# Kernel optimization log

Hardware: AMD Instinct MI355X
Metric: run time of the kernel (lower is better)

The kernel has to match this reference:

```python
import jax, jax.numpy as jnp
import numpy as np
from math import sqrt

B, S, E, H = 2, 2048, 768, 12
DH = E // H
W = 256            # one-sided attention window (attention_window=512)
G = 16             # number of global tokens (positions 0..G-1 in every batch row)
PAD = 128          # last PAD tokens per row are padding (masked)
FF = 3072          # SwiGLU intermediate size
NEG = -1e9
EPS = 1e-5


def _ln(x, g, b):
    m = jnp.mean(x, axis=-1, keepdims=True)
    v = jnp.var(x, axis=-1, keepdims=True)
    return (x - m) * jax.lax.rsqrt(v + EPS) * g + b


def _rope(x, t):
    # x: [B,H,S,DH]; t: [B,S] float 'set positions'
    half = DH // 2
    inv_freq = 1.0 / (10000.0 ** (jnp.arange(half, dtype=jnp.float32) / half))
    ang = t[:, None, :, None] * inv_freq            # [B,1,S,half]
    cos, sin = jnp.cos(ang), jnp.sin(ang)
    x1, x2 = x[..., :half], x[..., half:]
    return jnp.concatenate([x1 * cos - x2 * sin, x2 * cos + x1 * sin], axis=-1)


def _heads(x):  # [B,S,E] -> [B,H,S,DH]
    return x.reshape(B, S, H, DH).transpose(0, 2, 1, 3)


def _chunk3(x):
    # [B,H,S,D] -> [B,H,C,3W,D]: for query chunk c, keys from chunks c-1,c,c+1 (zero padded)
    b, h, s, d = x.shape
    c = s // W
    xp = jnp.pad(x, ((0, 0), (0, 0), (W, W), (0, 0))).reshape(b, h, c + 2, W, d)
    return jnp.concatenate([xp[:, :, :-2], xp[:, :, 1:-1], xp[:, :, 2:]], axis=3)


def _forward(x, attention_mask, global_attention_mask,
             Wq, bq, Wk, bk, Wv, bv, Wqg, bqg, Wkg, bkg, Wvg, bvg,
             ln0_g, ln0_b, ln1_g, ln1_b, W1, W3, W2):
    C = S // W
    merged = attention_mask * (global_attention_mask + 1)   # 0 masked, 1 local, 2 global
    is_masked = merged == 0
    is_global = merged == 2
    remove = merged != 1   # keys removed from windowed attention (masked or global)

    q = _heads(x @ Wq + bq) / sqrt(DH)
    k = _heads(x @ Wk + bk)
    v = _heads(x @ Wv + bv)

    # RoPE over 'set positions': (~is_index_masked) * cumsum(is_index_global_attn)
    t = jnp.where(is_masked, 0, jnp.cumsum(is_global.astype(jnp.int32), axis=1)).astype(jnp.float32)
    q = _rope(q, t)
    k = _rope(k, t)

    # --- sliding-window (banded) scores: band[b,h,i,d] = q_i . k_{i+d-W} ---
    qc = q.reshape(B, H, C, W, DH)
    k3 = _chunk3(k)
    s3 = jnp.einsum('bhcpd,bhcqd->bhcpq', qc, k3)                     # [B,H,C,W,3W]
    didx = jnp.arange(W)[:, None] + jnp.arange(2 * W + 1)[None, :]    # [W,2W+1]
    band = jnp.take_along_axis(s3, didx[None, None, None], axis=-1)   # [B,H,C,W,2W+1]

    # mask removed keys / out-of-range positions inside the band
    rmp = jnp.pad(remove, ((0, 0), (W, W)), constant_values=True).reshape(B, C + 2, W)
    rm3 = jnp.concatenate([rmp[:, :-2], rmp[:, 1:-1], rmp[:, 2:]], axis=2)  # [B,C,3W]
    band_rm = jnp.take_along_axis(jnp.broadcast_to(rm3[:, :, None, :], (B, C, W, 3 * W)),
                                  didx[None, None], axis=-1)                # [B,C,W,2W+1]
    band = jnp.where(band_rm[:, None], NEG, band).reshape(B, H, S, 2 * W + 1)

    # --- global-key columns (keys taken from the RoPE'd local key vectors) ---
    sg = jnp.einsum('bhid,bhgd->bhig', q, k[:, :, :G])                # [B,H,S,G]

    scores = jnp.concatenate([sg, band], axis=-1)                     # [B,H,S,G+2W+1]
    probs = jax.nn.softmax(scores.astype(jnp.float32), axis=-1).astype(x.dtype)
    probs = jnp.where(is_masked[:, None, :, None], 0.0, probs)

    # --- probs @ value: global columns + band ---
    out = jnp.einsum('bhig,bhgd->bhid', probs[..., :G], v[:, :, :G])
    pl = probs[..., G:].reshape(B, H, C, W, 2 * W + 1)
    rows = jnp.broadcast_to(jnp.arange(W)[:, None], (W, 2 * W + 1))
    p3 = jnp.zeros((B, H, C, W, 3 * W), probs.dtype).at[:, :, :, rows, didx].set(pl)
    v3 = _chunk3(v)
    out = out + jnp.einsum('bhcpq,bhcqd->bhcpd', p3, v3).reshape(B, H, S, DH)
    attn = out.transpose(0, 2, 1, 3).reshape(B, S, E)

    # --- full attention for global tokens (separate global projections, no RoPE) ---
    gq = _heads(x @ Wqg + bqg)[:, :, :G] / sqrt(DH)                   # [B,H,G,DH]
    gk = _heads(x @ Wkg + bkg)
    gv = _heads(x @ Wvg + bvg)
    gs = jnp.einsum('bhgd,bhjd->bhgj', gq, gk)                        # [B,H,G,S]
    gs = jnp.where(is_masked[:, None, None, :], NEG, gs)
    gp = jax.nn.softmax(gs.astype(jnp.float32), axis=-1).astype(x.dtype)
    gout = jnp.einsum('bhgj,bhjd->bhgd', gp, gv).transpose(0, 2, 1, 3).reshape(B, G, E)
    attn = attn.at[:, :G].set(gout)

    # residual + post-LN, SwiGLU FFN, residual + post-LN (dropout = eval mode)
    h0 = _ln(x + attn, ln0_g, ln0_b)
    ffn = (jax.nn.silu(h0 @ W1) * (h0 @ W3)) @ W2
    return _ln(h0 + ffn, ln1_g, ln1_b)


def setup_inputs():
    key = jax.random.key(0)
    ks = jax.random.split(key, 12)
    x = jax.random.normal(ks[0], (B, S, E), jnp.float32)
    attention_mask = jnp.ones((B, S), jnp.int32).at[:, S - PAD:].set(0)
    global_attention_mask = jnp.zeros((B, S), jnp.int32).at[:, :G].set(1)
    sd = 0.02
    def w(k, shape):
        return jax.random.normal(k, shape, jnp.float32) * sd
    return dict(
        x=x, attention_mask=attention_mask, global_attention_mask=global_attention_mask,
        Wq=w(ks[1], (E, E)), bq=jnp.zeros((E,), jnp.float32),
        Wk=w(ks[2], (E, E)), bk=jnp.zeros((E,), jnp.float32),
        Wv=w(ks[3], (E, E)), bv=jnp.zeros((E,), jnp.float32),
        Wqg=w(ks[4], (E, E)), bqg=jnp.zeros((E,), jnp.float32),
        Wkg=w(ks[5], (E, E)), bkg=jnp.zeros((E,), jnp.float32),
        Wvg=w(ks[6], (E, E)), bvg=jnp.zeros((E,), jnp.float32),
        ln0_g=jnp.ones((E,), jnp.float32), ln0_b=jnp.zeros((E,), jnp.float32),
        ln1_g=jnp.ones((E,), jnp.float32), ln1_b=jnp.zeros((E,), jnp.float32),
        W1=w(ks[7], (E, FF)), W3=w(ks[8], (E, FF)), W2=w(ks[9], (FF, E)))


def reference(x, attention_mask, global_attention_mask, Wq, bq, Wk, bk, Wv, bv,
              Wqg, bqg, Wkg, bkg, Wvg, bvg, ln0_g, ln0_b, ln1_g, ln1_b, W1, W3, W2):
    return _forward(x, attention_mask, global_attention_mask,
                    Wq, bq, Wk, bk, Wv, bv, Wqg, bqg, Wkg, bkg, Wvg, bvg,
                    ln0_g, ln0_b, ln1_g, ln1_b, W1, W3, W2)
```

## Files before the change

kernel.cpp:

```cpp
#include <hip/hip_runtime.h>


#define BB_ 2
#define SS 2048
#define EE 768
#define HH 12
#define DHH 64
#define GG 16
#define FFN 3072
#define MM (BB_*SS)

typedef __bf16 bf16_t;
typedef __bf16 bf16x8_t __attribute__((ext_vector_type(8)));
typedef float f32x4_t __attribute__((ext_vector_type(4)));

__device__ inline void gload16(const void* g, void* l) {
  __builtin_amdgcn_global_load_lds((const __attribute__((address_space(1))) void*)g,
                                   (__attribute__((address_space(3))) void*)l, 16, 0, 0);
}

__global__ __launch_bounds__(64) void detect_kernel(const unsigned int* __restrict__ w,
                                                    int* __restrict__ flag) {
  int cnt = 0;
  for (int i = threadIdx.x; i < 1024; i += 64) {
    unsigned e = (w[i] >> 7) & 0xFF;
    cnt += (e >= 100 && e <= 144) ? 1 : 0;
  }
  for (int off = 32; off; off >>= 1) cnt += __shfl_xor(cnt, off);
  if (threadIdx.x == 0) flag[0] = (cnt > 512) ? 1 : 0;
}

struct CanonP { const void* src[11]; bf16_t* dst[11]; };

__global__ __launch_bounds__(256) void canon_kernel(CanonP P, const int* __restrict__ flag) {
  constexpr int ns[11] = {3145728, 768,768,768,768,768,768, 768,768,768,768};
  int idx4 = (blockIdx.x*256 + threadIdx.x)*4;
  const bool isb = flag[0] != 0;
  int off = 0, seg = -1, loc = 0;
  #pragma unroll
  for (int i=0;i<11;i++) {
    if (seg < 0 && idx4 < off + ns[i]) { seg = i; loc = idx4 - off; }
    off += ns[i];
  }
  if (seg < 0) return;
  const void* s = P.src[seg];
  bf16_t* d = P.dst[seg];
  if (isb) {
    *(uint2*)&d[loc] = *(const uint2*)((const unsigned short*)s + loc);
  } else {
    float4 v = *(const float4*)((const float*)s + loc);
    d[loc+0] = (bf16_t)v.x; d[loc+1] = (bf16_t)v.y;
    d[loc+2] = (bf16_t)v.z; d[loc+3] = (bf16_t)v.w;
  }
}

struct TP6 { const void* s[6]; bf16_t* d[6]; };

__global__ __launch_bounds__(256) void trans_kernel(TP6 P, int R, int C,
                                                    const int* __restrict__ flag) {
  const int z = blockIdx.z;
  const void* src = P.s[z]; bf16_t* dst = P.d[z];
  const bool isb = flag[0] != 0;
  __shared__ bf16_t tile[32][33];
  int tx = threadIdx.x & 31, ty = threadIdx.x >> 5;
  int r0 = blockIdx.y*32, c0 = blockIdx.x*32;
  #pragma unroll
  for (int i=0;i<4;i++) {
    int rr = ty + i*8;
    size_t si = (size_t)(r0+rr)*C + c0 + tx;
    tile[rr][tx] = isb ? ((const bf16_t*)src)[si] : (bf16_t)((const float*)src)[si];
  }
  __syncthreads();
  #pragma unroll
  for (int i=0;i<4;i++) {
    int cc = ty + i*8;
    dst[(size_t)(c0+cc)*R + r0 + tx] = tile[tx][cc];
  }
}

__global__ __launch_bounds__(256) void flags_kernel(const int* __restrict__ am,
                                                    const int* __restrict__ gm,
                                                    float* __restrict__ tpos,
                                                    int* __restrict__ flags,
                                                    float* __restrict__ zbuf,
                                                    int zn) {
  int blk = blockIdx.x;
  if (blk >= BB_) {
    int i = (blk - BB_)*256 + threadIdx.x;
    if (i < zn) zbuf[i] = 0.f;
    return;
  }
  int b = blk;
  int t = threadIdx.x;
  int lane = t & 63, wv = t >> 6;
  int base = b*SS + t*8;
  int mg[8]; int isg[8]; int loc = 0;
  for (int i=0;i<8;i++) {
    int a = am[base+i], g = gm[base+i];
    int merged = a*(g+1);
    mg[i] = merged;
    isg[i] = (merged==2) ? 1 : 0;
    loc += isg[i];
  }
  int x = loc;
  for (int off=1; off<64; off<<=1) {
    int y = __shfl_up(x, off);
    if (lane >= off) x += y;
  }
  __shared__ int wtot[4];
  if (lane==63) wtot[wv] = x;
  __syncthreads();
  int prev = 0;
  for (int w=0; w<wv; w++) prev += wtot[w];
  int run = prev + x - loc;
  for (int i=0;i<8;i++) {
    run += isg[i];
    int masked = (mg[i]==0) ? 1 : 0;
    int glob   = (mg[i]==2) ? 1 : 0;
    int rem    = (mg[i]!=1) ? 1 : 0;
    tpos[base+i]  = masked ? 0.f : (float)run;
    flags[base+i] = masked | (glob<<1) | (rem<<2);
  }
}

__device__ inline void gemm128_core(const bf16_t* __restrict__ A,
                                    const bf16_t* __restrict__ BT,
                                    int ldA, int ldB, int kbeg, int kend,
                                    int m0, int n0,
                                    bf16_t* As, bf16_t* Bs,
                                    f32x4_t (&acc)[4][4]) {
  const int t = threadIdx.x;
  const int lane = t & 63, wv = t >> 6;
  const int l15 = lane & 15, quad = lane >> 4;
  const int wr = (wv >> 1) << 6, wc = (wv & 1) << 6;
  const int rsub = lane >> 3, pch = lane & 7;
  const int sch = pch ^ rsub;
  const size_t abase = (size_t)(m0 + wv*32 + rsub)*ldA + sch*8;
  const size_t bbase = (size_t)(n0 + wv*32 + rsub)*ldB + sch*8;
  const int sx = l15 & 7;
  bf16_t* lA = As + (wv*32)*64;
  bf16_t* lB = Bs + (wv*32)*64;
  for (int k0 = kbeg; k0 < kend; k0 += 64) {
    __syncthreads();
    #pragma unroll
    for (int j=0;j<4;j++) {
      gload16(A + abase + (size_t)(j*8)*ldA + k0, lA + j*8*64);
      gload16(BT + bbase + (size_t)(j*8)*ldB + k0, lB + j*8*64);
    }
    __syncthreads();
    #pragma unroll
    for (int c=0;c<2;c++) {
      bf16x8_t af[4], bfr[4];
      #pragma unroll
      for (int a=0;a<4;a++)
        af[a] = *(const bf16x8_t*)&As[(wr + a*16 + l15)*64 + ((c*4+quad)^sx)*8];
      #pragma unroll
      for (int b=0;b<4;b++)
        bfr[b] = *(const bf16x8_t*)&Bs[(wc + b*16 + l15)*64 + ((c*4+quad)^sx)*8];
      #pragma unroll
      for (int a=0;a<4;a++)
        #pragma unroll
        for (int b=0;b<4;b++)
          acc[a][b] = __builtin_amdgcn_mfma_f32_16x16x32_bf16(af[a], bfr[b], acc[a][b], 0,0,0);
    }
  }
}

struct ProjParams {
  const bf16_t* W[5];
  const bf16_t* Bi[5];
  bf16_t* O[5];
};

__global__ __launch_bounds__(256) void proj_kernel(const bf16_t* __restrict__ x,
                                                   ProjParams P,
                                                   const float* __restrict__ tpos) {
  const int m0 = blockIdx.x*128, n0 = blockIdx.y*128;
  const int z  = blockIdx.z;
  __shared__ bf16_t As[128*64];
  __shared__ bf16_t Bs[128*64];
  f32x4_t acc[4][4];
  #pragma unroll
  for (int a=0;a<4;a++)
    #pragma unroll
    for (int b=0;b<4;b++) acc[a][b] = (f32x4_t){0.f,0.f,0.f,0.f};
  gemm128_core(x, P.W[z], EE, EE, 0, EE, m0, n0, As, Bs, acc);

  const int t = threadIdx.x;
  const int lane = t & 63, wv = t >> 6;
  const int l15 = lane & 15, quad = lane >> 4;
  const int wr = (wv >> 1) << 6, wc = (wv & 1) << 6;
  const float scale = (z==0) ? 0.125f : 1.f;
  const bool rope = (z<2);
  const int h = (n0 + wc) >> 6;
  bf16_t* Oz = P.O[z];
  const bf16_t* Bz = P.Bi[z];
  float bvals[4];
  #pragma unroll
  for (int b=0;b<4;b++) bvals[b] = (float)Bz[h*64 + b*16 + l15];
  #pragma unroll
  for (int a=0;a<4;a++) {
    #pragma unroll
    for (int r=0;r<4;r++) {
      int row = m0 + wr + a*16 + quad*4 + r;
      int bb = row >> 11, spos = row & (SS-1);
      float vals[4];
      #pragma unroll
      for (int b=0;b<4;b++) vals[b] = (acc[a][b][r] + bvals[b]) * scale;
      if (rope) {
        float tv = tpos[row];
        #pragma unroll
        for (int b=0;b<2;b++) {
          int j = b*16 + l15;
          float inv = __expf(-(float)j * (9.210340371976184f/32.f));
          float ang = tv * inv;
          float sn = __sinf(ang), cs = __cosf(ang);
          float x1 = vals[b], x2 = vals[b+2];
          vals[b]   = x1*cs - x2*sn;
          vals[b+2] = x2*cs + x1*sn;
        }
      }
      bf16_t* dst = Oz + ((size_t)(bb*HH + h)*SS + spos)*DHH;
      #pragma unroll
      for (int b=0;b<4;b++) dst[b*16 + l15] = (bf16_t)vals[b];
    }
  }
}

__global__ __launch_bounds__(256) void gemm_ffn13(const bf16_t* __restrict__ A,
                                                  const bf16_t* __restrict__ B1T,
                                                  const bf16_t* __restrict__ B3T,
                                                  bf16_t* __restrict__ g1) {
  const int n0 = blockIdx.x*64, m0 = blockIdx.y*128;
  __shared__ bf16_t As[128*64];
  __shared__ bf16_t Bs1[64*64];
  __shared__ bf16_t Bs3[64*64];
  const int t = threadIdx.x;
  const int lane = t & 63, wv = t >> 6;
  const int l15 = lane & 15, quad = lane >> 4;
  const int wr = (wv >> 1) << 6, wc = (wv & 1) << 5;
  const int rsub = lane >> 3, pch = lane & 7;
  const int sch = pch ^ rsub;
  const size_t abase = (size_t)(m0 + wv*32 + rsub)*EE + sch*8;
  const size_t bbase = (size_t)(n0 + wv*16 + rsub)*EE + sch*8;
  const int sx = l15 & 7;
  bf16_t* lA  = As  + (wv*32)*64;
  bf16_t* lB1 = Bs1 + (wv*16)*64;
  bf16_t* lB3 = Bs3 + (wv*16)*64;
  f32x4_t a1[4][2], a3[4][2];
  #pragma unroll
  for (int a=0;a<4;a++)
    #pragma unroll
    for (int b=0;b<2;b++) { a1[a][b] = (f32x4_t){0.f,0.f,0.f,0.f};
                            a3[a][b] = (f32x4_t){0.f,0.f,0.f,0.f}; }
  for (int k0 = 0; k0 < EE; k0 += 64) {
    __syncthreads();
    #pragma unroll
    for (int j=0;j<4;j++)
      gload16(A + abase + (size_t)(j*8)*EE + k0, lA + j*8*64);
    #pragma unroll
    for (int j=0;j<2;j++) {
      gload16(B1T + bbase + (size_t)(j*8)*EE + k0, lB1 + j*8*64);
      gload16(B3T + bbase + (size_t)(j*8)*EE + k0, lB3 + j*8*64);
    }
    __syncthreads();
    #pragma unroll
    for (int c=0;c<2;c++) {
      bf16x8_t af[4], b1f[2], b3f[2];
      #pragma unroll
      for (int a=0;a<4;a++)
        af[a] = *(const bf16x8_t*)&As[(wr + a*16 + l15)*64 + ((c*4+quad)^sx)*8];
      #pragma unroll
      for (int b=0;b<2;b++) {
        b1f[b] = *(const bf16x8_t*)&Bs1[(wc + b*16 + l15)*64 + ((c*4+quad)^sx)*8];
        b3f[b] = *(const bf16x8_t*)&Bs3[(wc + b*16 + l15)*64 + ((c*4+quad)^sx)*8];
      }
      #pragma unroll
      for (int a=0;a<4;a++)
        #pragma unroll
        for (int b=0;b<2;b++) {
          a1[a][b] = __builtin_amdgcn_mfma_f32_16x16x32_bf16(af[a], b1f[b], a1[a][b], 0,0,0);
          a3[a][b] = __builtin_amdgcn_mfma_f32_16x16x32_bf16(af[a], b3f[b], a3[a][b], 0,0,0);
        }
    }
  }
  #pragma unroll
  for (int a=0;a<4;a++)
    #pragma unroll
    for (int r=0;r<4;r++) {
      int row = m0 + wr + a*16 + quad*4 + r;
      #pragma unroll
      for (int b=0;b<2;b++) {
        float tv = a1[a][b][r];
        float sil = tv / (1.f + __expf(-tv));
        g1[(size_t)row*FFN + n0 + wc + b*16 + l15] = (bf16_t)(sil * a3[a][b][r]);
      }
    }
}

struct Ffn2Out { float* p[4]; };

__global__ __launch_bounds__(256) void gemm_ffn2(const bf16_t* __restrict__ A,
                                                 const bf16_t* __restrict__ BT,
                                                 Ffn2Out O) {
  const int m0 = blockIdx.x*128, n0 = blockIdx.y*128;
  const int kz = blockIdx.z;
  __shared__ bf16_t As[128*64];
  __shared__ bf16_t Bs[128*64];
  f32x4_t acc[4][4];
  #pragma unroll
  for (int a=0;a<4;a++)
    #pragma unroll
    for (int b=0;b<4;b++) acc[a][b] = (f32x4_t){0.f,0.f,0.f,0.f};
  gemm128_core(A, BT, FFN, FFN, kz*768, (kz+1)*768, m0, n0, As, Bs, acc);
  const int t = threadIdx.x;
  const int lane = t & 63, wv = t >> 6;
  const int l15 = lane & 15, quad = lane >> 4;
  const int wr = (wv >> 1) << 6, wc = (wv & 1) << 6;
  float* C = O.p[kz];
  #pragma unroll
  for (int a=0;a<4;a++)
    #pragma unroll
    for (int r=0;r<4;r++) {
      int row = m0 + wr + a*16 + quad*4 + r;
      #pragma unroll
      for (int b=0;b<4;b++)
        C[(size_t)row*EE + n0 + wc + b*16 + l15] = acc[a][b][r];
    }
}

__global__ __launch_bounds__(64) void qg_kernel(const bf16_t* __restrict__ x,
                                                const bf16_t* __restrict__ WqgT,
                                                const bf16_t* __restrict__ bqg,
                                                float* __restrict__ qgb) {
  int g = blockIdx.x, h = blockIdx.y, b = blockIdx.z;
  int d = threadIdx.x;
  __shared__ float xs[EE];
  for (int i=d; i<EE; i+=64) xs[i] = (float)x[((size_t)b*SS + g)*EE + i];
  __syncthreads();
  float acc = 0.f;
  const bf16_t* wrow = WqgT + (size_t)(h*64+d)*EE;
  #pragma unroll 4
  for (int k=0;k<EE;k+=8) {
    bf16x8_t w8 = *(const bf16x8_t*)(wrow + k);
    #pragma unroll
    for (int i=0;i<8;i++) acc += xs[k+i] * (float)w8[i];
  }
  acc = (acc + (float)bqg[h*64+d]) * 0.125f;
  qgb[((size_t)(b*HH+h)*GG + g)*DHH + d] = acc;
}

__global__ __launch_bounds__(256) void band_kernel(const bf16_t* __restrict__ qb,
                                                   const bf16_t* __restrict__ kb,
                                                   const bf16_t* __restrict__ vb,
                                                   const int* __restrict__ flags,
                                                   float* __restrict__ attn) {
  const int flat = blockIdx.x;
  const int nb = (flat & 7) * 48 + (flat >> 3);
  const int px = nb & 15;
  const int hb = nb >> 4;
  const int h = hb % HH, b = hb / HH;
  const int p0 = px * 128;

  const int t = threadIdx.x;
  const int wv = t>>6, lane = t&63;
  const int l15 = lane & 15, quad = lane >> 4;
  const size_t bh = (size_t)(b*HH+h);
  const bf16_t* kbh = kb + bh*SS*DHH;
  const bf16_t* vbh = vb + bh*SS*DHH;
  const int* fl = flags + b*SS;
  const int qbase = p0 + wv*32;

  __shared__ bf16_t Ks[2][64*DHH];
  __shared__ bf16_t Vt[2][64*72];
  __shared__ bf16_t Pw[4][32*72];

  bf16x8_t qa[2][2];
  #pragma unroll
  for (int g=0; g<2; g++) {
    const bf16_t* qrow = qb + (bh*SS + qbase + g*16 + l15)*DHH;
    qa[g][0] = *(const bf16x8_t*)(qrow + quad*8);
    qa[g][1] = *(const bf16x8_t*)(qrow + 32 + quad*8);
  }

  const int srsub = lane >> 3, spch = lane & 7;
  const int vkp  = (t & 31) * 2;
  const int vdh0 = (t >> 5) * 8;

  {
    const int kb0 = p0 - 256;
    #pragma unroll
    for (int j=0;j<2;j++) {
      int row = wv*16 + j*8 + srsub;
      int kc = min(max(kb0 + row, 0), SS-1);
      gload16(kbh + (size_t)kc*DHH + (spch ^ srsub)*8, &Ks[0][(wv*16 + j*8)*DHH]);
    }
    int kc1 = min(max(kb0 + vkp,   0), SS-1);
    int kc2 = min(max(kb0 + vkp+1, 0), SS-1);
    bf16x8_t v1 = *(const bf16x8_t*)(vbh + (size_t)kc1*DHH + vdh0);
    bf16x8_t v2 = *(const bf16x8_t*)(vbh + (size_t)kc2*DHH + vdh0);
    #pragma unroll
    for (int i=0;i<8;i++) {
      union { unsigned u; bf16_t hh[2]; } pk;
      pk.hh[0] = v1[i]; pk.hh[1] = v2[i];
      *(unsigned*)&Vt[0][(vdh0+i)*72 + vkp] = pk.u;
    }
  }
  __syncthreads();

  f32x4_t o[2][4];
  #pragma unroll
  for (int g=0; g<2; g++)
    #pragma unroll
    for (int i=0;i<4;i++) o[g][i] = (f32x4_t){0.f,0.f,0.f,0.f};
  float lsum[2][4] = {{0.f,0.f,0.f,0.f},{0.f,0.f,0.f,0.f}};
  bf16_t* P = Pw[wv];

  for (int unit=0; unit<11; unit++) {
    const int cur = unit & 1, nxt = cur ^ 1;
    const int kb0 = (unit<10) ? (p0 - 256 + unit*64) : 0;
    const bool pre = (unit < 10);
    bf16x8_t pv1, pv2;
    if (pre) {
      const int kbn = (unit < 9) ? (kb0 + 64) : 0;
      #pragma unroll
      for (int j=0;j<2;j++) {
        int row = wv*16 + j*8 + srsub;
        int kc = min(max(kbn + row, 0), SS-1);
        gload16(kbh + (size_t)kc*DHH + (spch ^ srsub)*8, &Ks[nxt][(wv*16 + j*8)*DHH]);
      }
      int kc1 = min(max(kbn + vkp,   0), SS-1);
      int kc2 = min(max(kbn + vkp+1, 0), SS-1);
      pv1 = *(const bf16x8_t*)(vbh + (size_t)kc1*DHH + vdh0);
      pv2 = *(const bf16x8_t*)(vbh + (size_t)kc2*DHH + vdh0);
    }
    const bf16_t* Kc = Ks[cur];
    const int nsub = (unit<10) ? 4 : 1;
    for (int sub=0; sub<4; sub++) {
      if (sub < nsub) {
        int krow = sub*16 + l15;
        int kpos = kb0 + krow;
        bf16x8_t kf0 = *(const bf16x8_t*)&Kc[krow*DHH + (((quad  ) ^ (krow&7))<<3)];
        bf16x8_t kf1 = *(const bf16x8_t*)&Kc[krow*DHH + (((quad+4) ^ (krow&7))<<3)];
        int kc = min(max(kpos,0),SS-1);
        bool drop = false;
        if (unit<10) drop = (kpos<0) || (kpos>=SS) || (((fl[kc]>>2)&1)!=0);
        #pragma unroll
        for (int g=0; g<2; g++) {
          f32x4_t s = (f32x4_t){0.f,0.f,0.f,0.f};
          s = __builtin_amdgcn_mfma_f32_16x16x32_bf16(qa[g][0], kf0, s, 0,0,0);
          s = __builtin_amdgcn_mfma_f32_16x16x32_bf16(qa[g][1], kf1, s, 0,0,0);
          #pragma unroll
          for (int r=0;r<4;r++) {
            float e;
            if (unit==10) {
              e = __expf(s[r]);
            } else {
              int dj = kpos - (qbase + g*16 + quad*4 + r);
              bool valid = (dj>=-256) && (dj<=256) && (!drop);
              e = valid ? __expf(s[r]) : 0.f;
            }
            lsum[g][r] += e;
            P[(g*16 + quad*4 + r)*72 + sub*16 + l15] = (bf16_t)e;
          }
        }
      } else {
        #pragma unroll
        for (int g=0; g<2; g++)
          #pragma unroll
          for (int r=0;r<4;r++) P[(g*16 + quad*4 + r)*72 + sub*16 + l15] = (bf16_t)0.f;
      }
    }
    __builtin_amdgcn_s_setprio(1);
    #pragma unroll
    for (int g=0; g<2; g++) {
      #pragma unroll
      for (int chunk=0; chunk<2; chunk++) {
        bf16x8_t pf = *(const bf16x8_t*)&P[(g*16 + l15)*72 + chunk*32 + quad*8];
        #pragma unroll
        for (int nt=0; nt<4; nt++) {
          bf16x8_t vf = *(const bf16x8_t*)&Vt[cur][(nt*16+l15)*72 + chunk*32 + quad*8];
          o[g][nt] = __builtin_amdgcn_mfma_f32_16x16x32_bf16(pf, vf, o[g][nt], 0,0,0);
        }
      }
    }
    __builtin_amdgcn_s_setprio(0);
    if (pre) {
      #pragma unroll
      for (int i=0;i<8;i++) {
        union { unsigned u; bf16_t hh[2]; } pk;
        pk.hh[0] = pv1[i]; pk.hh[1] = pv2[i];
        *(unsigned*)&Vt[nxt][(vdh0+i)*72 + vkp] = pk.u;
      }
      __syncthreads();
    }
  }
  #pragma unroll
  for (int g=0; g<2; g++) {
    #pragma unroll
    for (int r=0;r<4;r++) {
      float s = lsum[g][r];
      s += __shfl_xor(s,1); s += __shfl_xor(s,2);
      s += __shfl_xor(s,4); s += __shfl_xor(s,8);
      lsum[g][r] = s;
    }
    #pragma unroll
    for (int r=0;r<4;r++) {
      int q = qbase + g*16 + quad*4 + r;
      int masked = fl[q] & 1;
      float inv = masked ? 0.f : 1.f/lsum[g][r];
      float* dst = attn + ((size_t)(b*SS+q))*EE + h*64 + l15;
      #pragma unroll
      for (int nt=0; nt<4; nt++) dst[nt*16] = o[g][nt][r]*inv;
    }
  }
}

__global__ __launch_bounds__(256) void gattn_part(const float* __restrict__ qgb,
                                                  const bf16_t* __restrict__ kgb,
                                                  const bf16_t* __restrict__ vgb,
                                                  const int* __restrict__ flags,
                                                  float* __restrict__ go,
                                                  float* __restrict__ gl) {
  const int kbase = blockIdx.x*128;
  const int h = blockIdx.y, b = blockIdx.z;
  const int t = threadIdx.x;
  __shared__ float gqs[16*68];
  __shared__ float Ks[64*68];
  __shared__ float Vs[64*68];
  __shared__ float es[16*64];
  const size_t bh = (size_t)(b*HH+h);
  #pragma unroll
  for (int j=0;j<4;j++) {
    int idx = t + j*256;
    int g = idx>>6, d = idx&63;
    gqs[g*68+d] = qgb[(bh*GG + g)*DHH + d];
  }
  float accv[4] = {0.f,0.f,0.f,0.f};
  float lpart = 0.f;
  const int gs = t>>4, kslot = t&15;
  const int dp = t&63, grp = t>>6;
  const bf16_t* kb_ = kgb + bh*SS*DHH;
  const bf16_t* vb_ = vgb + bh*SS*DHH;
  const int* fl = flags + b*SS;
  for (int tile=0; tile<2; tile++) {
    int k0 = kbase + tile*64;
    __syncthreads();
    {
      int row = t>>2, seg = t&3;
      const bf16_t* sk = kb_ + (size_t)(k0+row)*DHH + seg*16;
      const bf16_t* sv = vb_ + (size_t)(k0+row)*DHH + seg*16;
      bf16x8_t k1 = *(const bf16x8_t*)sk;
      bf16x8_t k2 = *(const bf16x8_t*)(sk+8);
      bf16x8_t v1 = *(const bf16x8_t*)sv;
      bf16x8_t v2 = *(const bf16x8_t*)(sv+8);
      #pragma unroll
      for (int i=0;i<8;i++) {
        Ks[row*68 + seg*16 + i]     = (float)k1[i];
        Ks[row*68 + seg*16 + 8 + i] = (float)k2[i];
        Vs[row*68 + seg*16 + i]     = (float)v1[i];
        Vs[row*68 + seg*16 + 8 + i] = (float)v2[i];
      }
    }
    __syncthreads();
    #pragma unroll
    for (int j=0;j<4;j++) {
      int key = kslot + 16*j;
      const float* gq = &gqs[gs*68];
      const float* kr = &Ks[key*68];
      float s = 0.f;
      #pragma unroll
      for (int d4=0; d4<64; d4+=4) {
        float4 a = *(const float4*)(gq + d4);
        float4 kk = *(const float4*)(kr + d4);
        s += a.x*kk.x + a.y*kk.y + a.z*kk.z + a.w*kk.w;
      }
      int msk = fl[k0+key] & 1;
      float e = msk ? 0.f : __expf(s);
      es[gs*64+key] = e;
      lpart += e;
    }
    __syncthreads();
    #pragma unroll
    for (int g=0; g<4; g++) {
      int gg = grp*4+g;
      float a = accv[g];
      for (int key=0;key<64;key++) a += es[gg*64+key]*Vs[key*68+dp];
      accv[g] = a;
    }
  }
  __syncthreads();
  es[gs*64 + kslot] = lpart;
  __syncthreads();
  if (t < 16) {
    float s = 0.f;
    for (int j=0;j<16;j++) s += es[t*64+j];
    atomicAdd(&gl[bh*16 + t], s);
  }
  #pragma unroll
  for (int g=0; g<4; g++)
    atomicAdd(&go[(bh*16 + grp*4+g)*64 + dp], accv[g]);
}

__global__ __launch_bounds__(256) void addln_kernel(const bf16_t* __restrict__ Abf,
                                                    const float* __restrict__ Af,
                                                    const float* __restrict__ B0,
                                                    const float* __restrict__ B1,
                                                    const float* __restrict__ B2,
                                                    const float* __restrict__ B3,
                                                    const float* __restrict__ gof,
                                                    const float* __restrict__ glf,
                                                    const bf16_t* __restrict__ gw,
                                                    const bf16_t* __restrict__ bw,
                                                    float* __restrict__ outf,
                                                    bf16_t* __restrict__ outb,
                                                    const int* __restrict__ flagp) {
  int r = blockIdx.x, t = threadIdx.x;
  int lane = t&63, wv = t>>6;
  int spos = r & (SS-1), bb = r >> 11;
  bool isglob = (gof != nullptr) && (spos < GG);
  float v[3]; float sum=0.f, ss=0.f;
  #pragma unroll
  for (int j=0;j<3;j++) {
    int idx = t + j*256;
    size_t gi = (size_t)r*EE+idx;
    float a = Abf ? (float)Abf[gi] : Af[gi];
    float bv;
    if (isglob) {
      int hh = idx >> 6, dp = idx & 63;
      int slot = (bb*HH + hh)*GG + spos;
      bv = gof[(size_t)slot*DHH + dp] / glf[slot];
    } else {
      bv = B0[gi];
    }
    float val = a + bv;
    if (B1) val += B1[gi];
    if (B2) val += B2[gi];
    if (B3) val += B3[gi];
    v[j] = val; sum += val; ss += val*val;
  }
  #pragma unroll
  for (int off=32; off>=1; off>>=1) {
    sum += __shfl_xor(sum, off);
    ss  += __shfl_xor(ss, off);
  }
  __shared__ float s1[4], s2[4];
  if (lane==0) { s1[wv]=sum; s2[wv]=ss; }
  __syncthreads();
  sum = s1[0]+s1[1]+s1[2]+s1[3];
  ss  = s2[0]+s2[1]+s2[2]+s2[3];
  float mean = sum * (1.f/(float)EE);
  float var  = ss * (1.f/(float)EE) - mean*mean;
  float rstd = rsqrtf(var + 1e-5f);
  bool wantb, wantf;
  if (flagp) { bool isb = (*flagp)!=0; wantb = isb; wantf = !isb; }
  else { wantb = (outb!=nullptr); wantf = (outf!=nullptr); }
  #pragma unroll
  for (int j=0;j<3;j++) {
    int idx = t + j*256;
    float o = (v[j]-mean)*rstd*(float)gw[idx] + (float)bw[idx];
    if (wantf) outf[(size_t)r*EE+idx] = o;
    if (wantb) outb[(size_t)r*EE+idx] = (bf16_t)o;
  }
}

extern "C" void kernel_launch(void* const* d_in, const int* in_sizes, int n_in,
                              void* d_out, int out_size, void* d_ws, size_t ws_size,
                              hipStream_t stream) {
  const void* x_r    = d_in[0];
  const int* am      = (const int*)d_in[1];
  const int* gm      = (const int*)d_in[2];
  (void)in_sizes; (void)n_in; (void)out_size; (void)ws_size;

  char* ws = (char*)d_ws;
  size_t off = 0;
  auto alloc = [&](size_t bytes) -> void* {
    void* p = ws + off;
    off += (bytes + 255) & ~(size_t)255;
    return p;
  };
  bf16_t* xc    = (bf16_t*)alloc((size_t)MM*EE*2);
  bf16_t* WT[6]; bf16_t* bc[6];
  for (int i=0;i<6;i++) { WT[i] = (bf16_t*)alloc((size_t)EE*EE*2); bc[i] = (bf16_t*)alloc(EE*2); }
  bf16_t* lnc[4];
  for (int i=0;i<4;i++) lnc[i] = (bf16_t*)alloc(EE*2);
  bf16_t* W1T = (bf16_t*)alloc((size_t)EE*FFN*2);
  bf16_t* W3T = (bf16_t*)alloc((size_t)EE*FFN*2);
  bf16_t* W2T = (bf16_t*)alloc((size_t)FFN*EE*2);
  const size_t NBHSD = (size_t)BB_*HH*SS*DHH;
  bf16_t* qb    = (bf16_t*)alloc(NBHSD*2);
  bf16_t* kb    = (bf16_t*)alloc(NBHSD*2);
  bf16_t* vb    = (bf16_t*)alloc(NBHSD*2);
  bf16_t* kgb   = (bf16_t*)alloc(NBHSD*2);
  bf16_t* vgb   = (bf16_t*)alloc(NBHSD*2);
  float* qgb   = (float*)alloc((size_t)BB_*HH*GG*DHH*4);
  float* attn  = (float*)alloc((size_t)MM*EE*4);
  float* h0f   = (float*)alloc((size_t)MM*EE*4);
  bf16_t* h0b  = (bf16_t*)alloc((size_t)MM*EE*2);
  bf16_t* g1   = (bf16_t*)alloc((size_t)MM*FFN*2);
  float* p3    = (float*)alloc((size_t)MM*EE*4);
  float* go    = (float*)alloc((size_t)BB_*HH*GG*DHH*4);
  float* gl    = (float*)alloc((size_t)BB_*HH*GG*4);
  float* tposb = (float*)alloc((size_t)BB_*SS*4);
  int*   flagb = (int*)alloc((size_t)BB_*SS*4);
  int*   dflag = (int*)alloc(256);
  float* p1 = (float*)qb;
  float* p2 = (float*)qb + (size_t)MM*EE;

  detect_kernel<<<1, 64, 0, stream>>>((const unsigned int*)d_in[3], dflag);

  CanonP CP;
  const void* csrc[11] = { x_r, d_in[4], d_in[6], d_in[8], d_in[10], d_in[12], d_in[14],
                           d_in[15], d_in[16], d_in[17], d_in[18] };
  bf16_t* cdst[11] = { xc, bc[0], bc[1], bc[2], bc[3], bc[4], bc[5],
                       lnc[0], lnc[1], lnc[2], lnc[3] };
  for (int i=0;i<11;i++) { CP.src[i]=csrc[i]; CP.dst[i]=cdst[i]; }
  canon_kernel<<<3081, 256, 0, stream>>>(CP, dflag);

  TP6 T6;
  const int wi[6] = {3,5,7,9,11,13};
  for (int i=0;i<6;i++) { T6.s[i]=d_in[wi[i]]; T6.d[i]=WT[i]; }
  trans_kernel<<<dim3(24,24,6), 256, 0, stream>>>(T6, EE, EE, dflag);
  TP6 TF; TF.s[0]=d_in[19]; TF.d[0]=W1T; TF.s[1]=d_in[20]; TF.d[1]=W3T;
  for (int i=2;i<6;i++) { TF.s[i]=d_in[19]; TF.d[i]=W1T; }
  trans_kernel<<<dim3(96,24,2), 256, 0, stream>>>(TF, EE, FFN, dflag);
  TP6 T2; T2.s[0]=d_in[21]; T2.d[0]=W2T;
  for (int i=1;i<6;i++) { T2.s[i]=d_in[21]; T2.d[i]=W2T; }
  trans_kernel<<<dim3(24,96,1), 256, 0, stream>>>(T2, FFN, EE, dflag);

  flags_kernel<<<BB_ + 98, 256, 0, stream>>>(am, gm, tposb, flagb, go, 24960);

  ProjParams P;
  P.W[0]=WT[0]; P.Bi[0]=bc[0]; P.O[0]=qb;
  P.W[1]=WT[1]; P.Bi[1]=bc[1]; P.O[1]=kb;
  P.W[2]=WT[2]; P.Bi[2]=bc[2]; P.O[2]=vb;
  P.W[3]=WT[4]; P.Bi[3]=bc[4]; P.O[3]=kgb;
  P.W[4]=WT[5]; P.Bi[4]=bc[5]; P.O[4]=vgb;
  proj_kernel<<<dim3(MM/128, EE/128, 5), 256, 0, stream>>>(xc, P, tposb);

  qg_kernel<<<dim3(GG, HH, BB_), 64, 0, stream>>>(xc, WT[3], bc[3], qgb);

  band_kernel<<<dim3(384), 256, 0, stream>>>(qb, kb, vb, flagb, attn);

  gattn_part<<<dim3(SS/128, HH, BB_), 256, 0, stream>>>(qgb, kgb, vgb, flagb, go, gl);

  addln_kernel<<<MM, 256, 0, stream>>>(xc, nullptr, attn, nullptr, nullptr, nullptr,
                                       go, gl, lnc[0], lnc[1], h0f, h0b, nullptr);

  gemm_ffn13<<<dim3(FFN/64, MM/128), 256, 0, stream>>>(h0b, W1T, W3T, g1);
  Ffn2Out FO; FO.p[0]=attn; FO.p[1]=p1; FO.p[2]=p2; FO.p[3]=p3;
  gemm_ffn2<<<dim3(MM/128, EE/128, 4), 256, 0, stream>>>(g1, W2T, FO);

  addln_kernel<<<MM, 256, 0, stream>>>(nullptr, h0f, attn, p1, p2, p3,
                                       nullptr, nullptr, lnc[2], lnc[3],
                                       (float*)d_out, (bf16_t*)d_out, dflag);
}
```

Before: 353.2 us.

## Merge prep, projection+global-query, and band+global attention into fused launches

Folds the canonicalisation, weight transposes and flag/zero kernels into a single prep kernel that dispatches on block index. It also merges the global-query projection into the projection GEMM launch and runs banded and global attention as one kernel with shared dynamic smem. The aim is to cut launch overhead and let independent small kernels fill idle CUs concurrently. The cost is larger shared-memory footprints per block, which may lower occupancy for the band part, and more branching per block.

```diff
diff --git a/kernel.cpp b/kernel.cpp
--- a/kernel.cpp
+++ b/kernel.cpp
@@ -30,97 +30,110 @@
   if (threadIdx.x == 0) flag[0] = (cnt > 512) ? 1 : 0;
 }
 
-struct CanonP { const void* src[11]; bf16_t* dst[11]; };
-
-__global__ __launch_bounds__(256) void canon_kernel(CanonP P, const int* __restrict__ flag) {
-  constexpr int ns[11] = {3145728, 768,768,768,768,768,768, 768,768,768,768};
-  int idx4 = (blockIdx.x*256 + threadIdx.x)*4;
+struct PrepParams {
+  const void* csrc[11]; bf16_t* cdst[11];
+  const void* tsrc[9];  bf16_t* tdst[9];
+  const int* am; const int* gm;
+  float* tpos; int* flags;
+  float* zbuf; int zn;
+};
+
+#define NB_CANON 3081
+#define NB_T1 3456
+#define NB_T2 4608
+#define NB_T3 2304
+#define NB_TRANS (NB_T1+NB_T2+NB_T3)
+
+__global__ __launch_bounds__(256) void prep_kernel(PrepParams P,
+                                                   const int* __restrict__ flag) {
+  __shared__ bf16_t tile[32][33];
+  __shared__ int wtot[4];
+  int bid = blockIdx.x;
+  const int t = threadIdx.x;
   const bool isb = flag[0] != 0;
-  int off = 0, seg = -1, loc = 0;
-  #pragma unroll
-  for (int i=0;i<11;i++) {
-    if (seg < 0 && idx4 < off + ns[i]) { seg = i; loc = idx4 - off; }
-    off += ns[i];
-  }
-  if (seg < 0) return;
-  const void* s = P.src[seg];
-  bf16_t* d = P.dst[seg];
-  if (isb) {
-    *(uint2*)&d[loc] = *(const uint2*)((const unsigned short*)s + loc);
-  } else {
-    float4 v = *(const float4*)((const float*)s + loc);
-    d[loc+0] = (bf16_t)v.x; d[loc+1] = (bf16_t)v.y;
-    d[loc+2] = (bf16_t)v.z; d[loc+3] = (bf16_t)v.w;
-  }
-}
-
-struct TP6 { const void* s[6]; bf16_t* d[6]; };
-
-__global__ __launch_bounds__(256) void trans_kernel(TP6 P, int R, int C,
-                                                    const int* __restrict__ flag) {
-  const int z = blockIdx.z;
-  const void* src = P.s[z]; bf16_t* dst = P.d[z];
-  const bool isb = flag[0] != 0;
-  __shared__ bf16_t tile[32][33];
-  int tx = threadIdx.x & 31, ty = threadIdx.x >> 5;
-  int r0 = blockIdx.y*32, c0 = blockIdx.x*32;
-  #pragma unroll
-  for (int i=0;i<4;i++) {
-    int rr = ty + i*8;
-    size_t si = (size_t)(r0+rr)*C + c0 + tx;
-    tile[rr][tx] = isb ? ((const bf16_t*)src)[si] : (bf16_t)((const float*)src)[si];
-  }
-  __syncthreads();
-  #pragma unroll
-  for (int i=0;i<4;i++) {
-    int cc = ty + i*8;
-    dst[(size_t)(c0+cc)*R + r0 + tx] = tile[tx][cc];
-  }
-}
-
-__global__ __launch_bounds__(256) void flags_kernel(const int* __restrict__ am,
-                                                    const int* __restrict__ gm,
-                                                    float* __restrict__ tpos,
-                                                    int* __restrict__ flags,
-                                                    float* __restrict__ zbuf,
-                                                    int zn) {
-  int blk = blockIdx.x;
-  if (blk >= BB_) {
-    int i = (blk - BB_)*256 + threadIdx.x;
-    if (i < zn) zbuf[i] = 0.f;
+
+  if (bid < NB_CANON) {
+    constexpr int ns[11] = {3145728, 768,768,768,768,768,768, 768,768,768,768};
+    int idx4 = (bid*256 + t)*4;
+    int off = 0, seg = -1, loc = 0;
+    #pragma unroll
+    for (int i=0;i<11;i++) {
+      if (seg < 0 && idx4 < off + ns[i]) { seg = i; loc = idx4 - off; }
+      off += ns[i];
+    }
+    if (seg < 0) return;
+    const void* s = P.csrc[seg];
+    bf16_t* d = P.cdst[seg];
+    if (isb) {
+      *(uint2*)&d[loc] = *(const uint2*)((const unsigned short*)s + loc);
+    } else {
+      float4 v = *(const float4*)((const float*)s + loc);
+      d[loc+0] = (bf16_t)v.x; d[loc+1] = (bf16_t)v.y;
+      d[loc+2] = (bf16_t)v.z; d[loc+3] = (bf16_t)v.w;
+    }
     return;
   }
-  int b = blk;
-  int t = threadIdx.x;
-  int lane = t & 63, wv = t >> 6;
-  int base = b*SS + t*8;
-  int mg[8]; int isg[8]; int loc = 0;
-  for (int i=0;i<8;i++) {
-    int a = am[base+i], g = gm[base+i];
-    int merged = a*(g+1);
-    mg[i] = merged;
-    isg[i] = (merged==2) ? 1 : 0;
-    loc += isg[i];
-  }
-  int x = loc;
-  for (int off=1; off<64; off<<=1) {
-    int y = __shfl_up(x, off);
-    if (lane >= off) x += y;
-  }
-  __shared__ int wtot[4];
-  if (lane==63) wtot[wv] = x;
-  __syncthreads();
-  int prev = 0;
-  for (int w=0; w<wv; w++) prev += wtot[w];
-  int run = prev + x - loc;
-  for (int i=0;i<8;i++) {
-    run += isg[i];
-    int masked = (mg[i]==0) ? 1 : 0;
-    int glob   = (mg[i]==2) ? 1 : 0;
-    int rem    = (mg[i]!=1) ? 1 : 0;
-    tpos[base+i]  = masked ? 0.f : (float)run;
-    flags[base+i] = masked | (glob<<1) | (rem<<2);
-  }
+  bid -= NB_CANON;
+
+  if (bid < NB_TRANS) {
+    int job, bx, by, R, C;
+    if (bid < NB_T1)            { job = bid/576;          int r = bid%576;  bx = r%24; by = r/24; R=EE;  C=EE;  }
+    else if (bid < NB_T1+NB_T2) { int l = bid-NB_T1; job = 6 + l/2304; int r = l%2304; bx = r%96; by = r/96; R=EE;  C=FFN; }
+    else                        { int l = bid-NB_T1-NB_T2; job = 8;          bx = l%24; by = l/24; R=FFN; C=EE;  }
+    const void* src = P.tsrc[job]; bf16_t* dst = P.tdst[job];
+    int tx = t & 31, ty = t >> 5;
+    int r0 = by*32, c0 = bx*32;
+    #pragma unroll
+    for (int i=0;i<4;i++) {
+      int rr = ty + i*8;
+      size_t si = (size_t)(r0+rr)*C + c0 + tx;
+      tile[rr][tx] = isb ? ((const bf16_t*)src)[si] : (bf16_t)((const float*)src)[si];
+    }
+    __syncthreads();
+    #pragma unroll
+    for (int i=0;i<4;i++) {
+      int cc = ty + i*8;
+      dst[(size_t)(c0+cc)*R + r0 + tx] = tile[tx][cc];
+    }
+    return;
+  }
+  bid -= NB_TRANS;
+
+  if (bid < BB_) {
+    int b = bid;
+    int lane = t & 63, wv = t >> 6;
+    int base = b*SS + t*8;
+    int mg[8]; int isg[8]; int loc = 0;
+    for (int i=0;i<8;i++) {
+      int a = P.am[base+i], g = P.gm[base+i];
+      int merged = a*(g+1);
+      mg[i] = merged;
+      isg[i] = (merged==2) ? 1 : 0;
+      loc += isg[i];
+    }
+    int x = loc;
+    for (int off=1; off<64; off<<=1) {
+      int y = __shfl_up(x, off);
+      if (lane >= off) x += y;
+    }
+    if (lane==63) wtot[wv] = x;
+    __syncthreads();
+    int prev = 0;
+    for (int w=0; w<wv; w++) prev += wtot[w];
+    int run = prev + x - loc;
+    for (int i=0;i<8;i++) {
+      run += isg[i];
+      int masked = (mg[i]==0) ? 1 : 0;
+      int glob   = (mg[i]==2) ? 1 : 0;
+      int rem    = (mg[i]!=1) ? 1 : 0;
+      P.tpos[base+i]  = masked ? 0.f : (float)run;
+      P.flags[base+i] = masked | (glob<<1) | (rem<<2);
+    }
+    return;
+  }
+  bid -= BB_;
+  int i = bid*256 + t;
+  if (i < P.zn) P.zbuf[i] = 0.f;
 }
 
 __device__ inline void gemm128_core(const bf16_t* __restrict__ A,
@@ -172,13 +185,43 @@
   bf16_t* O[5];
 };
 
-__global__ __launch_bounds__(256) void proj_kernel(const bf16_t* __restrict__ x,
-                                                   ProjParams P,
-                                                   const float* __restrict__ tpos) {
-  const int m0 = blockIdx.x*128, n0 = blockIdx.y*128;
-  const int z  = blockIdx.z;
+__global__ __launch_bounds__(256) void projqg_kernel(const bf16_t* __restrict__ x,
+                                                     ProjParams P,
+                                                     const float* __restrict__ tpos,
+                                                     const bf16_t* __restrict__ WqgT,
+                                                     const bf16_t* __restrict__ bqg,
+                                                     float* __restrict__ qgb) {
   __shared__ bf16_t As[128*64];
   __shared__ bf16_t Bs[128*64];
+  const int bid = blockIdx.x;
+  const int t = threadIdx.x;
+  const int lane = t & 63, wv = t >> 6;
+
+  if (bid >= 960) {
+    int l = bid - 960;
+    int g = l & 15;
+    int rest = l >> 4;
+    int hg = rest % 3, b = rest / 3;
+    float* xs = (float*)As;
+    for (int i=t; i<EE; i+=256) xs[i] = (float)x[((size_t)b*SS + g)*EE + i];
+    __syncthreads();
+    int h = hg*4 + wv, d = lane;
+    float acc = 0.f;
+    const bf16_t* wrow = WqgT + (size_t)(h*64+d)*EE;
+    #pragma unroll 4
+    for (int k=0;k<EE;k+=8) {
+      bf16x8_t w8 = *(const bf16x8_t*)(wrow + k);
+      #pragma unroll
+      for (int i=0;i<8;i++) acc += xs[k+i] * (float)w8[i];
+    }
+    acc = (acc + (float)bqg[h*64+d]) * 0.125f;
+    qgb[((size_t)(b*HH+h)*GG + g)*DHH + d] = acc;
+    return;
+  }
+
+  const int z  = bid / 192;
+  const int rem = bid % 192;
+  const int m0 = (rem % 32)*128, n0 = (rem / 32)*128;
   f32x4_t acc[4][4];
   #pragma unroll
   for (int a=0;a<4;a++)
@@ -186,8 +229,6 @@
     for (int b=0;b<4;b++) acc[a][b] = (f32x4_t){0.f,0.f,0.f,0.f};
   gemm128_core(x, P.W[z], EE, EE, 0, EE, m0, n0, As, Bs, acc);
 
-  const int t = threadIdx.x;
-  const int lane = t & 63, wv = t >> 6;
   const int l15 = lane & 15, quad = lane >> 4;
   const int wr = (wv >> 1) << 6, wc = (wv & 1) << 6;
   const float scale = (z==0) ? 0.125f : 1.f;
@@ -329,32 +370,12 @@
     }
 }
 
-__global__ __launch_bounds__(64) void qg_kernel(const bf16_t* __restrict__ x,
-                                                const bf16_t* __restrict__ WqgT,
-                                                const bf16_t* __restrict__ bqg,
-                                                float* __restrict__ qgb) {
-  int g = blockIdx.x, h = blockIdx.y, b = blockIdx.z;
-  int d = threadIdx.x;
-  __shared__ float xs[EE];
-  for (int i=d; i<EE; i+=64) xs[i] = (float)x[((size_t)b*SS + g)*EE + i];
-  __syncthreads();
-  float acc = 0.f;
-  const bf16_t* wrow = WqgT + (size_t)(h*64+d)*EE;
-  #pragma unroll 4
-  for (int k=0;k<EE;k+=8) {
-    bf16x8_t w8 = *(const bf16x8_t*)(wrow + k);
-    #pragma unroll
-    for (int i=0;i<8;i++) acc += xs[k+i] * (float)w8[i];
-  }
-  acc = (acc + (float)bqg[h*64+d]) * 0.125f;
-  qgb[((size_t)(b*HH+h)*GG + g)*DHH + d] = acc;
-}
-
-__global__ __launch_bounds__(256) void band_kernel(const bf16_t* __restrict__ qb,
-                                                   const bf16_t* __restrict__ kb,
-                                                   const bf16_t* __restrict__ vb,
-                                                   const int* __restrict__ flags,
-                                                   float* __restrict__ attn) {
+__device__ void band_body(char* smem,
+                          const bf16_t* __restrict__ qb,
+                          const bf16_t* __restrict__ kb,
+                          const bf16_t* __restrict__ vb,
+                          const int* __restrict__ flags,
+                          float* __restrict__ attn) {
   const int flat = blockIdx.x;
   const int nb = (flat & 7) * 48 + (flat >> 3);
   const int px = nb & 15;
@@ -371,9 +392,9 @@
   const int* fl = flags + b*SS;
   const int qbase = p0 + wv*32;
 
-  __shared__ bf16_t Ks[2][64*DHH];
-  __shared__ bf16_t Vt[2][64*72];
-  __shared__ bf16_t Pw[4][32*72];
+  bf16_t* KsB = (bf16_t*)smem;
+  bf16_t* VtB = (bf16_t*)(smem + 16384);
+  bf16_t* PwB = (bf16_t*)(smem + 35840);
 
   bf16x8_t qa[2][2];
   #pragma unroll
@@ -393,7 +414,7 @@
     for (int j=0;j<2;j++) {
       int row = wv*16 + j*8 + srsub;
       int kc = min(max(kb0 + row, 0), SS-1);
-      gload16(kbh + (size_t)kc*DHH + (spch ^ srsub)*8, &Ks[0][(wv*16 + j*8)*DHH]);
+      gload16(kbh + (size_t)kc*DHH + (spch ^ srsub)*8, &KsB[(wv*16 + j*8)*DHH]);
     }
     int kc1 = min(max(kb0 + vkp,   0), SS-1);
     int kc2 = min(max(kb0 + vkp+1, 0), SS-1);
@@ -403,7 +424,7 @@
     for (int i=0;i<8;i++) {
       union { unsigned u; bf16_t hh[2]; } pk;
       pk.hh[0] = v1[i]; pk.hh[1] = v2[i];
-      *(unsigned*)&Vt[0][(vdh0+i)*72 + vkp] = pk.u;
+      *(unsigned*)&VtB[(vdh0+i)*72 + vkp] = pk.u;
     }
   }
   __syncthreads();
@@ -414,7 +435,7 @@
     #pragma unroll
     for (int i=0;i<4;i++) o[g][i] = (f32x4_t){0.f,0.f,0.f,0.f};
   float lsum[2][4] = {{0.f,0.f,0.f,0.f},{0.f,0.f,0.f,0.f}};
-  bf16_t* P = Pw[wv];
+  bf16_t* P = PwB + wv*(32*72);
 
   for (int unit=0; unit<11; unit++) {
     const int cur = unit & 1, nxt = cur ^ 1;
@@ -427,14 +448,15 @@
       for (int j=0;j<2;j++) {
         int row = wv*16 + j*8 + srsub;
         int kc = min(max(kbn + row, 0), SS-1);
-        gload16(kbh + (size_t)kc*DHH + (spch ^ srsub)*8, &Ks[nxt][(wv*16 + j*8)*DHH]);
+        gload16(kbh + (size_t)kc*DHH + (spch ^ srsub)*8,
+                &KsB[nxt*(64*DHH) + (wv*16 + j*8)*DHH]);
       }
       int kc1 = min(max(kbn + vkp,   0), SS-1);
       int kc2 = min(max(kbn + vkp+1, 0), SS-1);
       pv1 = *(const bf16x8_t*)(vbh + (size_t)kc1*DHH + vdh0);
       pv2 = *(const bf16x8_t*)(vbh + (size_t)kc2*DHH + vdh0);
     }
-    const bf16_t* Kc = Ks[cur];
+    const bf16_t* Kc = KsB + cur*(64*DHH);
     const int nsub = (unit<10) ? 4 : 1;
     for (int sub=0; sub<4; sub++) {
       if (sub < nsub) {
@@ -471,6 +493,7 @@
           for (int r=0;r<4;r++) P[(g*16 + quad*4 + r)*72 + sub*16 + l15] = (bf16_t)0.f;
       }
     }
+    const bf16_t* Vc = VtB + cur*(64*72);
     __builtin_amdgcn_s_setprio(1);
     #pragma unroll
     for (int g=0; g<2; g++) {
@@ -479,7 +502,7 @@
         bf16x8_t pf = *(const bf16x8_t*)&P[(g*16 + l15)*72 + chunk*32 + quad*8];
         #pragma unroll
         for (int nt=0; nt<4; nt++) {
-          bf16x8_t vf = *(const bf16x8_t*)&Vt[cur][(nt*16+l15)*72 + chunk*32 + quad*8];
+          bf16x8_t vf = *(const bf16x8_t*)&Vc[(nt*16+l15)*72 + chunk*32 + quad*8];
           o[g][nt] = __builtin_amdgcn_mfma_f32_16x16x32_bf16(pf, vf, o[g][nt], 0,0,0);
         }
       }
@@ -490,7 +513,7 @@
       for (int i=0;i<8;i++) {
         union { unsigned u; bf16_t hh[2]; } pk;
         pk.hh[0] = pv1[i]; pk.hh[1] = pv2[i];
-        *(unsigned*)&Vt[nxt][(vdh0+i)*72 + vkp] = pk.u;
+        *(unsigned*)&VtB[nxt*(64*72) + (vdh0+i)*72 + vkp] = pk.u;
       }
       __syncthreads();
     }
@@ -516,19 +539,21 @@
   }
 }
 
-__global__ __launch_bounds__(256) void gattn_part(const float* __restrict__ qgb,
-                                                  const bf16_t* __restrict__ kgb,
-                                                  const bf16_t* __restrict__ vgb,
-                                                  const int* __restrict__ flags,
-                                                  float* __restrict__ go,
-                                                  float* __restrict__ gl) {
-  const int kbase = blockIdx.x*128;
-  const int h = blockIdx.y, b = blockIdx.z;
+__device__ void gattn_body(char* smem,
+                           const float* __restrict__ qgb,
+                           const bf16_t* __restrict__ kgb,
+                           const bf16_t* __restrict__ vgb,
+                           const int* __restrict__ flags,
+                           float* __restrict__ go,
+                           float* __restrict__ gl) {
+  const int l = blockIdx.x - 384;
+  const int kbase = (l % 16)*128;
+  const int h = (l / 16) % HH, b = l / (16*HH);
   const int t = threadIdx.x;
-  __shared__ float gqs[16*68];
-  __shared__ float Ks[64*68];
-  __shared__ float Vs[64*68];
-  __shared__ float es[16*64];
+  float* gqs = (float*)smem;
+  float* Ks  = gqs + 16*68;
+  float* Vs  = Ks + 64*68;
+  float* es  = Vs + 64*68;
   const size_t bh = (size_t)(b*HH+h);
   #pragma unroll
   for (int j=0;j<4;j++) {
@@ -600,6 +625,21 @@
   #pragma unroll
   for (int g=0; g<4; g++)
     atomicAdd(&go[(bh*16 + grp*4+g)*64 + dp], accv[g]);
+}
+
+__global__ __launch_bounds__(256) void attn_kernel(const bf16_t* __restrict__ qb,
+                                                   const bf16_t* __restrict__ kb,
+                                                   const bf16_t* __restrict__ vb,
+                                                   const float* __restrict__ qgb,
+                                                   const bf16_t* __restrict__ kgb,
+                                                   const bf16_t* __restrict__ vgb,
+                                                   const int* __restrict__ flags,
+                                                   float* __restrict__ attn,
+                                                   float* __restrict__ go,
+                                                   float* __restrict__ gl) {
+  __shared__ __align__(16) char smem[54272];
+  if (blockIdx.x < 384) band_body(smem, qb, kb, vb, flags, attn);
+  else                  gattn_body(smem, qgb, kgb, vgb, flags, go, gl);
 }
 
 __global__ __launch_bounds__(256) void addln_kernel(const bf16_t* __restrict__ Abf,
@@ -709,26 +749,20 @@
 
   detect_kernel<<<1, 64, 0, stream>>>((const unsigned int*)d_in[3], dflag);
 
-  CanonP CP;
+  PrepParams PP;
   const void* csrc[11] = { x_r, d_in[4], d_in[6], d_in[8], d_in[10], d_in[12], d_in[14],
                            d_in[15], d_in[16], d_in[17], d_in[18] };
   bf16_t* cdst[11] = { xc, bc[0], bc[1], bc[2], bc[3], bc[4], bc[5],
                        lnc[0], lnc[1], lnc[2], lnc[3] };
-  for (int i=0;i<11;i++) { CP.src[i]=csrc[i]; CP.dst[i]=cdst[i]; }
-  canon_kernel<<<3081, 256, 0, stream>>>(CP, dflag);
-
-  TP6 T6;
+  for (int i=0;i<11;i++) { PP.csrc[i]=csrc[i]; PP.cdst[i]=cdst[i]; }
   const int wi[6] = {3,5,7,9,11,13};
-  for (int i=0;i<6;i++) { T6.s[i]=d_in[wi[i]]; T6.d[i]=WT[i]; }
-  trans_kernel<<<dim3(24,24,6), 256, 0, stream>>>(T6, EE, EE, dflag);
-  TP6 TF; TF.s[0]=d_in[19]; TF.d[0]=W1T; TF.s[1]=d_in[20]; TF.d[1]=W3T;
-  for (int i=2;i<6;i++) { TF.s[i]=d_in[19]; TF.d[i]=W1T; }
-  trans_kernel<<<dim3(96,24,2), 256, 0, stream>>>(TF, EE, FFN, dflag);
-  TP6 T2; T2.s[0]=d_in[21]; T2.d[0]=W2T;
-  for (int i=1;i<6;i++) { T2.s[i]=d_in[21]; T2.d[i]=W2T; }
-  trans_kernel<<<dim3(24,96,1), 256, 0, stream>>>(T2, FFN, EE, dflag);
-
-  flags_kernel<<<BB_ + 98, 256, 0, stream>>>(am, gm, tposb, flagb, go, 24960);
+  for (int i=0;i<6;i++) { PP.tsrc[i]=d_in[wi[i]]; PP.tdst[i]=WT[i]; }
+  PP.tsrc[6]=d_in[19]; PP.tdst[6]=W1T;
+  PP.tsrc[7]=d_in[20]; PP.tdst[7]=W3T;
+  PP.tsrc[8]=d_in[21]; PP.tdst[8]=W2T;
+  PP.am = am; PP.gm = gm; PP.tpos = tposb; PP.flags = flagb;
+  PP.zbuf = go; PP.zn = 24960;
+  prep_kernel<<<NB_CANON + NB_TRANS + BB_ + 98, 256, 0, stream>>>(PP, dflag);
 
   ProjParams P;
   P.W[0]=WT[0]; P.Bi[0]=bc[0]; P.O[0]=qb;
@@ -736,13 +770,10 @@
   P.W[2]=WT[2]; P.Bi[2]=bc[2]; P.O[2]=vb;
   P.W[3]=WT[4]; P.Bi[3]=bc[4]; P.O[3]=kgb;
   P.W[4]=WT[5]; P.Bi[4]=bc[5]; P.O[4]=vgb;
-  proj_kernel<<<dim3(MM/128, EE/128, 5), 256, 0, stream>>>(xc, P, tposb);
-
-  qg_kernel<<<dim3(GG, HH, BB_), 64, 0, stream>>>(xc, WT[3], bc[3], qgb);
-
-  band_kernel<<<dim3(384), 256, 0, stream>>>(qb, kb, vb, flagb, attn);
-
-  gattn_part<<<dim3(SS/128, HH, BB_), 256, 0, stream>>>(qgb, kgb, vgb, flagb, go, gl);
+  projqg_kernel<<<dim3(1056), 256, 0, stream>>>(xc, P, tposb, WT[3], bc[3], qgb);
+
+  attn_kernel<<<dim3(768), 256, 0, stream>>>(qb, kb, vb, qgb, kgb, vgb,
+                                             flagb, attn, go, gl);
 
   addln_kernel<<<MM, 256, 0, stream>>>(xc, nullptr, attn, nullptr, nullptr, nullptr,
                                        go, gl, lnc[0], lnc[1], h0f, h0b, nullptr);
```

Result: no change. 347.7 us (-1.6%).
